# Performance work log

Measured on AMD Instinct MI355X. Metric: run time of the kernel, lower is better.

The kernel has to match this reference:

```python
import jax, jax.numpy as jnp
import numpy as np

B, T, I, H = 256, 2048, 128, 128

def setup_inputs() -> dict:
    key = jax.random.key(0)
    k = jax.random.split(key, 5)
    bound = 1.0 / np.sqrt(H)  # torch RNNCell init: U(-1/sqrt(H), 1/sqrt(H))
    return {
        "x": jax.random.normal(k[0], (B, T, I), dtype=jnp.float32),
        "weight_ih": jax.random.uniform(k[1], (H, I), jnp.float32, -bound, bound),
        "weight_hh": jax.random.uniform(k[2], (H, H), jnp.float32, -bound, bound),
        "bias_ih": jax.random.uniform(k[3], (H,), jnp.float32, -bound, bound),
        "bias_hh": jax.random.uniform(k[4], (H,), jnp.float32, -bound, bound),
    }

def reference(x, weight_ih, weight_hh, bias_ih, bias_hh):
    # Tanh RNN: h_t = tanh(x_t @ W_ih^T + b_ih + h_{t-1} @ W_hh^T + b_hh)
    # Precompute the input projection for all timesteps (one big GEMM),
    # then scan the recurrent part (sequential dependency on h).
    b = x.shape[0]
    h0 = jnp.zeros((b, weight_hh.shape[0]), dtype=x.dtype)
    # [B, T, H]
    x_proj = jnp.einsum('bti,hi->bth', x, weight_ih) + bias_ih + bias_hh

    def step(h, xt):  # xt: [B, H]
        h_new = jnp.tanh(xt + h @ weight_hh.T)
        return h_new, h_new

    _, out = jax.lax.scan(step, h0, jnp.swapaxes(x_proj, 0, 1))  # out: [T, B, H]
    return jnp.swapaxes(out, 0, 1)  # [B, T, H]
```

## Files before the change

kernel.cpp:

```cpp
#include <hip/hip_runtime.h>

#define BB 256
#define TT 2048
#define II 128
#define HH 128
#define GS 16
#define NG (TT / GS)

typedef __attribute__((ext_vector_type(8))) short short8;
typedef __attribute__((ext_vector_type(4))) float f32x4;

__device__ __forceinline__ void step_barrier() {
    asm volatile("s_waitcnt lgkmcnt(0)\n\ts_barrier" ::: "memory");
}

__device__ __forceinline__ float tanh_fast(float s) {
#if __has_builtin(__builtin_amdgcn_exp2f)
    const float e = __builtin_amdgcn_exp2f(s * 2.8853900817779268f);
#else
    const float e = exp2f(s * 2.8853900817779268f);
#endif
    return 1.0f - 2.0f * __builtin_amdgcn_rcpf(e + 1.0f);
}

__device__ __forceinline__ unsigned int f2bf(float f) {
    unsigned int u = __float_as_uint(f);
    u += 0x7FFF + ((u >> 16) & 1);
    return u >> 16;
}
__device__ __forceinline__ unsigned int pack2(float lo, float hi) {
    return f2bf(lo) | (f2bf(hi) << 16);
}

__launch_bounds__(512, 1)
__global__ void rnn_pipe(const float* __restrict__ x,
                         const float* __restrict__ w_ih,
                         const float* __restrict__ w_hh,
                         const float* __restrict__ b_ih,
                         const float* __restrict__ b_hh,
                         float* __restrict__ out) {
    const int b    = blockIdx.x;
    const int tid  = threadIdx.x;
    const int wave = tid >> 6;
    const int lane = tid & 63;
    const bool hw  = (wave < 4);

    __shared__ __align__(16) unsigned short hA[2][HH];
    __shared__ __align__(16) float axbuf[2][GS][HH];
    __shared__ __align__(16) unsigned short xstage[2][4][64][8];

    const float* xb = x + (size_t)b * (TT * II);
    const f32x4 z4 = {0.f, 0.f, 0.f, 0.f};

    const int jb_h = (wave & 3) * 32;
    short8 WH[2][4];
    if (hw) {
#pragma unroll
        for (int nt = 0; nt < 2; ++nt) {
            const int jj = jb_h + nt * 16 + (lane & 15);
#pragma unroll
            for (int kf = 0; kf < 4; ++kf) {
                short8 s;
#pragma unroll
                for (int e = 0; e < 8; ++e) {
                    const int kp = kf * 32 + (lane >> 4) * 8 + e;
                    const int mm = kp & 31;
                    const int ko = (kp & ~31) + (mm >> 1) + ((mm & 1) << 4);
                    s[e] = (short)f2bf(w_hh[(size_t)jj * HH + ko]);
                }
                WH[nt][kf] = s;
            }
        }
    }

    const int xwq = wave - 4;
    const int jb  = xwq * 32;
    short8 WF[2][4];
    float biasv[2];
    f32x4 bs0 = z4, bs1 = z4;
    const int q   = tid - 256;
    const int t_s = q >> 4;
    const int m   = q & 15;
    const int i0  = m * 8;
    const int kfs = m >> 2;
    const int lps = (m & 3) * 16 + t_s;
    if (!hw) {
#pragma unroll
        for (int nt = 0; nt < 2; ++nt) {
            const int jj = jb + nt * 16 + (lane & 15);
            biasv[nt] = b_ih[jj] + b_hh[jj];
#pragma unroll
            for (int kf = 0; kf < 4; ++kf) {
                const float* wp = w_ih + (size_t)jj * II + kf * 32 + (lane >> 4) * 8;
                short8 s;
#pragma unroll
                for (int e = 0; e < 8; ++e) s[e] = (short)f2bf(wp[e]);
                WF[nt][kf] = s;
            }
        }
#pragma unroll
        for (int r = 0; r < 4; ++r) { bs0[r] = biasv[0]; bs1[r] = biasv[1]; }
    }

#define STAGE_X(BUF, R0, R1) do { \
        uint4 P_; P_.x = pack2((R0).x, (R0).y); P_.y = pack2((R0).z, (R0).w); \
        P_.z = pack2((R1).x, (R1).y); P_.w = pack2((R1).z, (R1).w); \
        *reinterpret_cast<uint4*>(&xstage[BUF][kfs][lps][0]) = P_; } while (0)

#define XPROJ(SB, AB) do { \
        const short8 PA0 = *reinterpret_cast<const short8*>(&xstage[SB][0][lane][0]); \
        const short8 PA1 = *reinterpret_cast<const short8*>(&xstage[SB][1][lane][0]); \
        const short8 PA2 = *reinterpret_cast<const short8*>(&xstage[SB][2][lane][0]); \
        const short8 PA3 = *reinterpret_cast<const short8*>(&xstage[SB][3][lane][0]); \
        f32x4 ac0 = z4, ac1 = z4; \
        ac0 = __builtin_amdgcn_mfma_f32_16x16x32_bf16(PA0, WF[0][0], ac0, 0, 0, 0); \
        ac0 = __builtin_amdgcn_mfma_f32_16x16x32_bf16(PA1, WF[0][1], ac0, 0, 0, 0); \
        ac0 = __builtin_amdgcn_mfma_f32_16x16x32_bf16(PA2, WF[0][2], ac0, 0, 0, 0); \
        ac0 = __builtin_amdgcn_mfma_f32_16x16x32_bf16(PA3, WF[0][3], ac0, 0, 0, 0); \
        ac1 = __builtin_amdgcn_mfma_f32_16x16x32_bf16(PA0, WF[1][0], ac1, 0, 0, 0); \
        ac1 = __builtin_amdgcn_mfma_f32_16x16x32_bf16(PA1, WF[1][1], ac1, 0, 0, 0); \
        ac1 = __builtin_amdgcn_mfma_f32_16x16x32_bf16(PA2, WF[1][2], ac1, 0, 0, 0); \
        ac1 = __builtin_amdgcn_mfma_f32_16x16x32_bf16(PA3, WF[1][3], ac1, 0, 0, 0); \
        const int c_ = lane & 15, rb_ = (lane >> 4) * 4; \
        _Pragma("unroll") \
        for (int r = 0; r < 4; ++r) { \
            axbuf[AB][rb_ + r][jb + c_]      = ac0[r] + biasv[0]; \
            axbuf[AB][rb_ + r][jb + 16 + c_] = ac1[r] + biasv[1]; \
        } } while (0)

    float4 nr0, nr1;
    if (!hw) {
        float4 p0 = *reinterpret_cast<const float4*>(&xb[t_s * II + i0]);
        float4 p1 = *reinterpret_cast<const float4*>(&xb[t_s * II + i0 + 4]);
        STAGE_X(1, p0, p1);
        nr0 = *reinterpret_cast<const float4*>(&xb[(GS + t_s) * II + i0]);
        nr1 = *reinterpret_cast<const float4*>(&xb[(GS + t_s) * II + i0 + 4]);
    }
    if (tid < HH) hA[0][tid] = 0;
    __syncthreads();
    if (!hw) {
        XPROJ(1, 0);
        STAGE_X(0, nr0, nr1);
    }
    __syncthreads();

    const int c16 = lane & 15;
    float axn0 = 0.f, axn1 = 0.f;
    f32x4 d00 = z4, d10 = z4;
    float* ob = out + (size_t)b * (TT * HH) + jb_h + lane;
    if (hw) {
        axn0 = axbuf[0][0][jb_h + c16];
        axn1 = axbuf[0][0][jb_h + 16 + c16];
    }

    short8 XA0 = {}, XA1 = {}, XA2 = {}, XA3 = {};
    f32x4 xp0 = z4, xp1 = z4, xp2 = z4, xp3 = z4;
    f32x4 yp0 = z4, yp1 = z4, yp2 = z4, yp3 = z4;

    for (int g = 0; g < NG; ++g) {
#pragma unroll
        for (int w = 0; w < GS; ++w) {
            if (hw) {
                const int p  = w & 1;
                const int ko = (lane >> 4) * 8;
                const short8 A0 = *reinterpret_cast<const short8*>(&hA[p][ 0 + ko]);
                const short8 A1 = *reinterpret_cast<const short8*>(&hA[p][32 + ko]);
                const short8 A2 = *reinterpret_cast<const short8*>(&hA[p][64 + ko]);
                const short8 A3 = *reinterpret_cast<const short8*>(&hA[p][96 + ko]);
                d00[0] = axn0;
                d10[0] = axn1;
                f32x4 e01, e02, e03, e11, e12, e13;
                d00 = __builtin_amdgcn_mfma_f32_16x16x32_bf16(A0, WH[0][0], d00, 0, 0, 0);
                e01 = __builtin_amdgcn_mfma_f32_16x16x32_bf16(A1, WH[0][1], z4,  0, 0, 0);
                e02 = __builtin_amdgcn_mfma_f32_16x16x32_bf16(A2, WH[0][2], z4,  0, 0, 0);
                e03 = __builtin_amdgcn_mfma_f32_16x16x32_bf16(A3, WH[0][3], z4,  0, 0, 0);
                d10 = __builtin_amdgcn_mfma_f32_16x16x32_bf16(A0, WH[1][0], d10, 0, 0, 0);
                e11 = __builtin_amdgcn_mfma_f32_16x16x32_bf16(A1, WH[1][1], z4,  0, 0, 0);
                e12 = __builtin_amdgcn_mfma_f32_16x16x32_bf16(A2, WH[1][2], z4,  0, 0, 0);
                e13 = __builtin_amdgcn_mfma_f32_16x16x32_bf16(A3, WH[1][3], z4,  0, 0, 0);
                {
                    const int wn  = (w + 1) & (GS - 1);
                    const int gnb = (w == GS - 1) ? ((g + 1) & 1) : (g & 1);
                    axn0 = axbuf[gnb][wn][jb_h + c16];
                    axn1 = axbuf[gnb][wn][jb_h + 16 + c16];
                }
                const float s0 = (d00[0] + e01[0]) + (e02[0] + e03[0]);
                const float s1 = (d10[0] + e11[0]) + (e12[0] + e13[0]);
                const float hn0 = tanh_fast(s0);
                const float hn1 = tanh_fast(s1);
                if (lane < 16) {
                    *reinterpret_cast<unsigned int*>(&hA[p ^ 1][jb_h + 2 * lane])
                        = pack2(hn0, hn1);
                    ob[0]  = hn0;
                    ob[16] = hn1;
                }
                ob += HH;
            } else {
                if (w == 0 && g + 1 < NG) {
                    XA0 = *reinterpret_cast<const short8*>(&xstage[g & 1][0][lane][0]);
                    XA1 = *reinterpret_cast<const short8*>(&xstage[g & 1][1][lane][0]);
                    XA2 = *reinterpret_cast<const short8*>(&xstage[g & 1][2][lane][0]);
                    XA3 = *reinterpret_cast<const short8*>(&xstage[g & 1][3][lane][0]);
                }
                if (w == 1 && g + 2 < NG) {
                    const int tb = (g + 2) * GS;
                    nr0 = *reinterpret_cast<const float4*>(&xb[(size_t)(tb + t_s) * II + i0]);
                    nr1 = *reinterpret_cast<const float4*>(&xb[(size_t)(tb + t_s) * II + i0 + 4]);
                }
                if (g + 1 < NG) {
                    if (w == 1) xp0 = __builtin_amdgcn_mfma_f32_16x16x32_bf16(XA0, WF[0][0], bs0, 0, 0, 0);
                    if (w == 2) yp0 = __builtin_amdgcn_mfma_f32_16x16x32_bf16(XA0, WF[1][0], bs1, 0, 0, 0);
                    if (w == 3) xp1 = __builtin_amdgcn_mfma_f32_16x16x32_bf16(XA1, WF[0][1], z4, 0, 0, 0);
                    if (w == 4) yp1 = __builtin_amdgcn_mfma_f32_16x16x32_bf16(XA1, WF[1][1], z4, 0, 0, 0);
                    if (w == 5) xp2 = __builtin_amdgcn_mfma_f32_16x16x32_bf16(XA2, WF[0][2], z4, 0, 0, 0);
                    if (w == 6) yp2 = __builtin_amdgcn_mfma_f32_16x16x32_bf16(XA2, WF[1][2], z4, 0, 0, 0);
                    if (w == 7) xp3 = __builtin_amdgcn_mfma_f32_16x16x32_bf16(XA3, WF[0][3], z4, 0, 0, 0);
                    if (w == 8) yp3 = __builtin_amdgcn_mfma_f32_16x16x32_bf16(XA3, WF[1][3], z4, 0, 0, 0);
                    if (w == 9) {
                        const f32x4 t0 = (xp0 + xp1) + (xp2 + xp3);
                        const f32x4 t1 = (yp0 + yp1) + (yp2 + yp3);
                        const int c_ = lane & 15, rb_ = (lane >> 4) * 4;
#pragma unroll
                        for (int r = 0; r < 4; ++r) {
                            axbuf[(g + 1) & 1][rb_ + r][jb + c_]      = t0[r];
                            axbuf[(g + 1) & 1][rb_ + r][jb + 16 + c_] = t1[r];
                        }
                    }
                }
                if (w == 11 && g + 2 < NG) {
                    STAGE_X((g + 1) & 1, nr0, nr1);
                }
            }
            step_barrier();
        }
    }
#undef XPROJ
#undef STAGE_X
}

extern "C" void kernel_launch(void* const* d_in, const int* in_sizes, int n_in,
                              void* d_out, int out_size, void* d_ws, size_t ws_size,
                              hipStream_t stream) {
    const float* x    = (const float*)d_in[0];
    const float* w_ih = (const float*)d_in[1];
    const float* w_hh = (const float*)d_in[2];
    const float* b_ih = (const float*)d_in[3];
    const float* b_hh = (const float*)d_in[4];
    float* out = (float*)d_out;

    rnn_pipe<<<BB, 512, 0, stream>>>(x, w_ih, w_hh, b_ih, b_hh, out);
}
```

Before: 512.6 us.

## Deepen x-projection pipeline to triple-buffered axbuf, batching projection work in one step

The input-projection buffer grows from double to triple buffering, and the prologue precomputes two groups up front. The projection waves now do all their MFMAs, LDS staging and global prefetch in a single step (w==14), one group further ahead, instead of spreading them across steps. The aim is to hide global-load latency better and reduce per-step branching on the projection waves. In exchange it uses more LDS and adds modulo-3 indexing on the recurrent path, and bunching the work into one step could lengthen that step's barrier wait.

```diff
diff --git a/kernel.cpp b/kernel.cpp
--- a/kernel.cpp
+++ b/kernel.cpp
@@ -46,7 +46,7 @@
     const bool hw  = (wave < 4);
 
     __shared__ __align__(16) unsigned short hA[2][HH];
-    __shared__ __align__(16) float axbuf[2][GS][HH];
+    __shared__ __align__(16) float axbuf[3][GS][HH];
     __shared__ __align__(16) unsigned short xstage[2][4][64][8];
 
     const float* xb = x + (size_t)b * (TT * II);
@@ -132,15 +132,26 @@
     if (!hw) {
         float4 p0 = *reinterpret_cast<const float4*>(&xb[t_s * II + i0]);
         float4 p1 = *reinterpret_cast<const float4*>(&xb[t_s * II + i0 + 4]);
-        STAGE_X(1, p0, p1);
-        nr0 = *reinterpret_cast<const float4*>(&xb[(GS + t_s) * II + i0]);
-        nr1 = *reinterpret_cast<const float4*>(&xb[(GS + t_s) * II + i0 + 4]);
+        STAGE_X(0, p0, p1);
     }
     if (tid < HH) hA[0][tid] = 0;
     __syncthreads();
-    if (!hw) {
-        XPROJ(1, 0);
-        STAGE_X(0, nr0, nr1);
+    if (!hw) XPROJ(0, 0);
+    __syncthreads();
+    if (!hw) {
+        float4 p0 = *reinterpret_cast<const float4*>(&xb[(GS + t_s) * II + i0]);
+        float4 p1 = *reinterpret_cast<const float4*>(&xb[(GS + t_s) * II + i0 + 4]);
+        STAGE_X(0, p0, p1);
+    }
+    __syncthreads();
+    if (!hw) XPROJ(0, 1);
+    __syncthreads();
+    if (!hw) {
+        float4 p0 = *reinterpret_cast<const float4*>(&xb[(2 * GS + t_s) * II + i0]);
+        float4 p1 = *reinterpret_cast<const float4*>(&xb[(2 * GS + t_s) * II + i0 + 4]);
+        STAGE_X(0, p0, p1);
+        nr0 = *reinterpret_cast<const float4*>(&xb[(size_t)(3 * GS + t_s) * II + i0]);
+        nr1 = *reinterpret_cast<const float4*>(&xb[(size_t)(3 * GS + t_s) * II + i0 + 4]);
     }
     __syncthreads();
 
@@ -153,11 +164,10 @@
         axn1 = axbuf[0][0][jb_h + 16 + c16];
     }
 
-    short8 XA0 = {}, XA1 = {}, XA2 = {}, XA3 = {};
-    f32x4 xp0 = z4, xp1 = z4, xp2 = z4, xp3 = z4;
-    f32x4 yp0 = z4, yp1 = z4, yp2 = z4, yp3 = z4;
-
     for (int g = 0; g < NG; ++g) {
+        const int g3  = g % 3;
+        const int g3n = (g + 1) % 3;
+        const int g3x = (g + 2) % 3;
 #pragma unroll
         for (int w = 0; w < GS; ++w) {
             if (hw) {
@@ -180,7 +190,7 @@
                 e13 = __builtin_amdgcn_mfma_f32_16x16x32_bf16(A3, WH[1][3], z4,  0, 0, 0);
                 {
                     const int wn  = (w + 1) & (GS - 1);
-                    const int gnb = (w == GS - 1) ? ((g + 1) & 1) : (g & 1);
+                    const int gnb = (w == GS - 1) ? g3n : g3;
                     axn0 = axbuf[gnb][wn][jb_h + c16];
                     axn1 = axbuf[gnb][wn][jb_h + 16 + c16];
                 }
@@ -195,40 +205,37 @@
                     ob[16] = hn1;
                 }
                 ob += HH;
-            } else {
-                if (w == 0 && g + 1 < NG) {
-                    XA0 = *reinterpret_cast<const short8*>(&xstage[g & 1][0][lane][0]);
-                    XA1 = *reinterpret_cast<const short8*>(&xstage[g & 1][1][lane][0]);
-                    XA2 = *reinterpret_cast<const short8*>(&xstage[g & 1][2][lane][0]);
-                    XA3 = *reinterpret_cast<const short8*>(&xstage[g & 1][3][lane][0]);
-                }
-                if (w == 1 && g + 2 < NG) {
-                    const int tb = (g + 2) * GS;
+            } else if (w == 14) {
+                if (g + 2 < NG) {
+                    const short8 XA0 = *reinterpret_cast<const short8*>(&xstage[g & 1][0][lane][0]);
+                    const short8 XA1 = *reinterpret_cast<const short8*>(&xstage[g & 1][1][lane][0]);
+                    const short8 XA2 = *reinterpret_cast<const short8*>(&xstage[g & 1][2][lane][0]);
+                    const short8 XA3 = *reinterpret_cast<const short8*>(&xstage[g & 1][3][lane][0]);
+                    f32x4 xp0, xp1, xp2, xp3, yp0, yp1, yp2, yp3;
+                    xp0 = __builtin_amdgcn_mfma_f32_16x16x32_bf16(XA0, WF[0][0], bs0, 0, 0, 0);
+                    yp0 = __builtin_amdgcn_mfma_f32_16x16x32_bf16(XA0, WF[1][0], bs1, 0, 0, 0);
+                    xp1 = __builtin_amdgcn_mfma_f32_16x16x32_bf16(XA1, WF[0][1], z4, 0, 0, 0);
+                    yp1 = __builtin_amdgcn_mfma_f32_16x16x32_bf16(XA1, WF[1][1], z4, 0, 0, 0);
+                    xp2 = __builtin_amdgcn_mfma_f32_16x16x32_bf16(XA2, WF[0][2], z4, 0, 0, 0);
+                    yp2 = __builtin_amdgcn_mfma_f32_16x16x32_bf16(XA2, WF[1][2], z4, 0, 0, 0);
+                    xp3 = __builtin_amdgcn_mfma_f32_16x16x32_bf16(XA3, WF[0][3], z4, 0, 0, 0);
+                    yp3 = __builtin_amdgcn_mfma_f32_16x16x32_bf16(XA3, WF[1][3], z4, 0, 0, 0);
+                    const f32x4 t0 = (xp0 + xp1) + (xp2 + xp3);
+                    const f32x4 t1 = (yp0 + yp1) + (yp2 + yp3);
+                    const int c_ = lane & 15, rb_ = (lane >> 4) * 4;
+#pragma unroll
+                    for (int r = 0; r < 4; ++r) {
+                        axbuf[g3x][rb_ + r][jb + c_]      = t0[r];
+                        axbuf[g3x][rb_ + r][jb + 16 + c_] = t1[r];
+                    }
+                }
+                if (g + 3 < NG) {
+                    STAGE_X((g + 1) & 1, nr0, nr1);
+                }
+                if (g + 4 < NG) {
+                    const int tb = (g + 4) * GS;
                     nr0 = *reinterpret_cast<const float4*>(&xb[(size_t)(tb + t_s) * II + i0]);
                     nr1 = *reinterpret_cast<const float4*>(&xb[(size_t)(tb + t_s) * II + i0 + 4]);
-                }
-                if (g + 1 < NG) {
-                    if (w == 1) xp0 = __builtin_amdgcn_mfma_f32_16x16x32_bf16(XA0, WF[0][0], bs0, 0, 0, 0);
-                    if (w == 2) yp0 = __builtin_amdgcn_mfma_f32_16x16x32_bf16(XA0, WF[1][0], bs1, 0, 0, 0);
-                    if (w == 3) xp1 = __builtin_amdgcn_mfma_f32_16x16x32_bf16(XA1, WF[0][1], z4, 0, 0, 0);
-                    if (w == 4) yp1 = __builtin_amdgcn_mfma_f32_16x16x32_bf16(XA1, WF[1][1], z4, 0, 0, 0);
-                    if (w == 5) xp2 = __builtin_amdgcn_mfma_f32_16x16x32_bf16(XA2, WF[0][2], z4, 0, 0, 0);
-                    if (w == 6) yp2 = __builtin_amdgcn_mfma_f32_16x16x32_bf16(XA2, WF[1][2], z4, 0, 0, 0);
-                    if (w == 7) xp3 = __builtin_amdgcn_mfma_f32_16x16x32_bf16(XA3, WF[0][3], z4, 0, 0, 0);
-                    if (w == 8) yp3 = __builtin_amdgcn_mfma_f32_16x16x32_bf16(XA3, WF[1][3], z4, 0, 0, 0);
-                    if (w == 9) {
-                        const f32x4 t0 = (xp0 + xp1) + (xp2 + xp3);
-                        const f32x4 t1 = (yp0 + yp1) + (yp2 + yp3);
-                        const int c_ = lane & 15, rb_ = (lane >> 4) * 4;
-#pragma unroll
-                        for (int r = 0; r < 4; ++r) {
-                            axbuf[(g + 1) & 1][rb_ + r][jb + c_]      = t0[r];
-                            axbuf[(g + 1) & 1][rb_ + r][jb + 16 + c_] = t1[r];
-                        }
-                    }
-                }
-                if (w == 11 && g + 2 < NG) {
-                    STAGE_X((g + 1) & 1, nr0, nr1);
                 }
             }
             step_barrier();
```

Result: no change. 502.6 us (-1.9%).
